# Optimization experiments

Measured on AMD Instinct MI355X. Metric: run time of the kernel, lower is better.

The kernel has to match this reference:

```python
import jax, jax.numpy as jnp
import numpy as np

B, K, N, F_IN, F_OUT, T = 8, 3, 2048, 16, 64, 12


def setup_inputs() -> dict:
    key = jax.random.key(0)
    k1, k2, k3, k4 = jax.random.split(key, 4)
    x = jax.random.normal(k1, (B, N, F_IN, T), dtype=jnp.float32)
    spatial_attention = jax.random.normal(k2, (B, K, N, N), dtype=jnp.float32)
    adj = jax.random.uniform(k3, (N, N), dtype=jnp.float32)  # fusiongraph() output
    Theta = jax.random.normal(k4, (K, F_IN, F_OUT), dtype=jnp.float32) * 0.1
    return {"x": x, "spatial_attention": spatial_attention, "adj": adj, "Theta": Theta}


def _cheb_polynomials(L_tilde, k_order):
    # NOTE: original uses ELEMENTWISE multiply in the recurrence (L_tilde * T_{k-1}),
    # faithfully reproduced here.
    n = L_tilde.shape[0]
    polys = [jnp.eye(n, dtype=L_tilde.dtype), L_tilde]
    for _ in range(2, k_order):
        polys.append(2.0 * L_tilde * polys[-1] - polys[-2])
    return jnp.stack(polys[:k_order], axis=0)  # (K, N, N)


def reference(x, spatial_attention, adj, Theta):
    # Unnormalized graph Laplacian L = D - A (torch_geometric get_laplacian default).
    deg = jnp.sum(adj, axis=1)                      # (N,)
    L_tilde = jnp.diag(deg) - adj                   # (N, N)
    cheb = _cheb_polynomials(L_tilde, K)            # (K, N, N)

    # softmax over dim=1 of each (B,N,N) slice -> axis=2 of (B,K,N,N); time-invariant.
    attn = jax.nn.softmax(spatial_attention, axis=2)  # (B, K, N, N)
    Tka = cheb[None, :, :, :] * attn                  # (B, K, N, N)

    # rhs[b,n,f,t] = sum_m Tka[b,k,m,n] * x[b,m,f,t]; out = rhs @ Theta_k, summed over k.
    out = jnp.einsum('bkmn,bmft,kfo->bnot', Tka, x, Theta)  # (B, N, F_OUT, T)
    return jax.nn.relu(out)
```

## Files before the change

kernel.cpp:

```cpp
#include <hip/hip_runtime.h>


#define NB 8
#define NN 2048
#define FT 192
#define BN 32
#define BM 64
#define LBM 72
#define ZST 33

typedef __attribute__((ext_vector_type(8))) short short8;
typedef __attribute__((ext_vector_type(4))) float f32x4;

__device__ __forceinline__ unsigned short bf16_rne(float f) {
  unsigned u = __float_as_uint(f);
  u += 0x7FFFu + ((u >> 16) & 1u);
  return (unsigned short)(u >> 16);
}

__device__ __forceinline__ void gload_lds16(const float* g, float* l) {
  __builtin_amdgcn_global_load_lds(
      (const __attribute__((address_space(1))) void*)g,
      (__attribute__((address_space(3))) void*)l, 16, 0, 0);
}

__global__ __launch_bounds__(256) void k_deg(const float* __restrict__ adj,
                                             float* __restrict__ deg) {
  const int row = blockIdx.x;
  const float* r = adj + (size_t)row * NN;
  float s = 0.f;
  for (int j = threadIdx.x; j < NN; j += 256) s += r[j];
  for (int off = 32; off; off >>= 1) s += __shfl_down(s, off, 64);
  __shared__ float ls[4];
  if ((threadIdx.x & 63) == 0) ls[threadIdx.x >> 6] = s;
  __syncthreads();
  if (threadIdx.x == 0) deg[row] = ls[0] + ls[1] + ls[2] + ls[3];
}

__global__ __launch_bounds__(192) void k_xt(const float* __restrict__ x,
                                            unsigned short* __restrict__ xT) {
  const int b = blockIdx.y, m0 = blockIdx.x * 32, ft = threadIdx.x;
  const float* src = x + (size_t)b * NN * FT + ft;
  uint4* dst = (uint4*)(xT + ((size_t)b * FT + ft) * NN + m0);
#pragma unroll
  for (int g = 0; g < 4; ++g) {
    unsigned u[4];
#pragma unroll
    for (int j = 0; j < 4; ++j) {
      float lo = src[(size_t)(m0 + g * 8 + 2 * j) * FT];
      float hi = src[(size_t)(m0 + g * 8 + 2 * j + 1) * FT];
      u[j] = (unsigned)bf16_rne(lo) | ((unsigned)bf16_rne(hi) << 16);
    }
    dst[g] = make_uint4(u[0], u[1], u[2], u[3]);
  }
}

__global__ __launch_bounds__(256, 2) void k_fused(
    const float* __restrict__ Sall, const float* __restrict__ adj,
    const float* __restrict__ deg, const unsigned short* __restrict__ xT,
    const float* __restrict__ x, const float* __restrict__ Theta,
    float* __restrict__ out) {
  __shared__ __align__(16) char smem[74752];
  __shared__ float dEs[BN];
  __shared__ float sc[3][BN];

  float* const Sr1 = (float*)smem;
  float* const Sr2 = (float*)(smem + 8192);
  unsigned short* const PtB = (unsigned short*)(smem + 16384);

  const int flat = blockIdx.x + (blockIdx.y << 6);
  const int b = flat & 7;
  const int tile = flat >> 3;
  const int n0 = tile * BN;

  const int t = threadIdx.x;
  const int lane = t & 63, w = t >> 6;
  const int ln = lane & 15, quad = lane >> 4;
  const int col4 = (t & 7) << 2;
  const int rowg = t >> 3;
  const int srow = lane >> 3;
  const int scol = (lane & 7) << 2;

  const float* S0 = Sall + (size_t)b * 3 * NN * NN;
  const float* S1 = S0 + (size_t)NN * NN;
  const float* S2 = S1 + (size_t)NN * NN;
  const unsigned short* xb = xT + (size_t)b * FT * NN;

  const int cdiag = n0 >> 6;
  const float4 dgv = *(const float4*)(deg + n0 + col4);

  const f32x4 zero4 = {0.f, 0.f, 0.f, 0.f};
  f32x4 acc1[2][3], acc2[2][3];
#pragma unroll
  for (int i = 0; i < 2; ++i)
#pragma unroll
    for (int q = 0; q < 3; ++q) {
      acc1[i][q] = zero4;
      acc2[i][q] = zero4;
    }
  float zp0[4] = {0.f, 0.f, 0.f, 0.f};
  float zp1[4] = {0.f, 0.f, 0.f, 0.f};
  float zp2[4] = {0.f, 0.f, 0.f, 0.f};

  auto STAGE = [&](int c) {
    const int m0s = c * BM;
#pragma unroll
    for (int j2 = 0; j2 < 2; ++j2) {
      const int r0 = (w << 4) + (j2 << 3);
      const size_t go = (size_t)(m0s + r0 + srow) * NN + n0 + scol;
      gload_lds16(S1 + go, Sr1 + r0 * BN);
      gload_lds16(S2 + go, Sr2 + r0 * BN);
    }
  };

  auto LOADAV = [&](int c, float4 av[2], float4 sv[2]) {
#pragma unroll
    for (int r = 0; r < 2; ++r) {
      const int gm = c * BM + rowg * 2 + r;
      av[r] = *(const float4*)(adj + (size_t)gm * NN + n0 + col4);
      sv[r] = *(const float4*)(S0 + (size_t)gm * NN + n0 + col4);
    }
  };

  auto PACK = [&](int c, int buf, const float4 av[2], const float4 sv[2]) {
    const bool isd = (c == cdiag);
    unsigned short* P1 = PtB + (size_t)buf * 2304;
    unsigned short* P2 = PtB + (size_t)(2 + buf) * 2304;
    unsigned short q1[2][4], q2[2][4];
    const float dg[4] = {dgv.x, dgv.y, dgv.z, dgv.w};
#pragma unroll
    for (int r = 0; r < 2; ++r) {
      const int lrow = rowg * 2 + r;
      const float4 s1 = *(const float4*)&Sr1[lrow * BN + col4];
      const float4 s2 = *(const float4*)&Sr2[lrow * BN + col4];
      const float se1[4] = {s1.x, s1.y, s1.z, s1.w};
      const float se2[4] = {s2.x, s2.y, s2.z, s2.w};
      const float aa[4] = {av[r].x, av[r].y, av[r].z, av[r].w};
      const float s0e[4] = {sv[r].x, sv[r].y, sv[r].z, sv[r].w};
#pragma unroll
      for (int j = 0; j < 4; ++j) {
        const float e0 = __expf(s0e[j]);
        const float e1 = __expf(se1[j]);
        const float e2 = __expf(se2[j]);
        zp0[j] += e0;
        zp1[j] += e1;
        zp2[j] += e2;
        float c1 = -aa[j];
        float c2 = 2.f * aa[j] * aa[j];
        if (isd) {
          if (c * BM + lrow == n0 + col4 + j) {
            const float L = dg[j] - aa[j];
            c1 = L;
            c2 = 2.f * L * L - 1.f;
            dEs[col4 + j] = e0;
          }
        }
        q1[r][j] = bf16_rne(e1 * c1);
        q2[r][j] = bf16_rne(e2 * c2);
      }
    }
#pragma unroll
    for (int j = 0; j < 4; ++j) {
      const unsigned v1 = (unsigned)q1[0][j] | ((unsigned)q1[1][j] << 16);
      const unsigned v2 = (unsigned)q2[0][j] | ((unsigned)q2[1][j] << 16);
      *(unsigned*)&P1[(col4 + j) * LBM + rowg * 2] = v1;
      *(unsigned*)&P2[(col4 + j) * LBM + rowg * 2] = v2;
    }
  };

  STAGE(0);
  {
    float4 av[2], sv[2];
    LOADAV(0, av, sv);
    asm volatile("s_waitcnt vmcnt(0)" ::: "memory");
    __builtin_amdgcn_sched_barrier(0);
    PACK(0, 0, av, sv);
  }
  __syncthreads();

  for (int c = 0; c < 32; ++c) {
    const int buf = c & 1;
    const bool more = (c < 31);
    const int m0 = c * BM;

    short8 bfr[2][3];
#pragma unroll
    for (int ks2 = 0; ks2 < 2; ++ks2)
#pragma unroll
      for (int q = 0; q < 3; ++q)
        bfr[ks2][q] = *(const short8*)(xb +
            (size_t)(w * 48 + q * 16 + ln) * NN + m0 + ks2 * 32 + quad * 8);
    __builtin_amdgcn_sched_barrier(0);

    float4 avn[2], svn[2];
    if (more) {
      STAGE(c + 1);
      LOADAV(c + 1, avn, svn);
    }
    __builtin_amdgcn_sched_barrier(0);

#pragma unroll
    for (int ks2 = 0; ks2 < 2; ++ks2) {
      short8 a1[2], a2[2];
#pragma unroll
      for (int i = 0; i < 2; ++i) {
        a1[i] = *(const short8*)&PtB[(size_t)buf * 2304 + (i * 16 + ln) * LBM +
                                     ks2 * 32 + quad * 8];
        a2[i] = *(const short8*)&PtB[(size_t)(2 + buf) * 2304 +
                                     (i * 16 + ln) * LBM + ks2 * 32 + quad * 8];
      }
#pragma unroll
      for (int i = 0; i < 2; ++i)
#pragma unroll
        for (int q = 0; q < 3; ++q) {
          acc1[i][q] = __builtin_amdgcn_mfma_f32_16x16x32_bf16(
              a1[i], bfr[ks2][q], acc1[i][q], 0, 0, 0);
          acc2[i][q] = __builtin_amdgcn_mfma_f32_16x16x32_bf16(
              a2[i], bfr[ks2][q], acc2[i][q], 0, 0, 0);
        }
    }

    if (more) {
      asm volatile("s_waitcnt vmcnt(0)" ::: "memory");
      __builtin_amdgcn_sched_barrier(0);
      PACK(c + 1, buf ^ 1, avn, svn);
    }
    __syncthreads();
  }

  float* Zr = (float*)smem;
#pragma unroll
  for (int j = 0; j < 4; ++j) {
    Zr[0 * 32 * ZST + rowg * ZST + col4 + j] = zp0[j];
    Zr[1 * 32 * ZST + rowg * ZST + col4 + j] = zp1[j];
    Zr[2 * 32 * ZST + rowg * ZST + col4 + j] = zp2[j];
  }
  __syncthreads();
  if (t < 96) {
    const int which = t >> 5, n = t & 31;
    float Z = 0.f;
#pragma unroll
    for (int g = 0; g < 32; ++g) Z += Zr[which * 32 * ZST + g * ZST + n];
    sc[which][n] = (which == 0) ? (dEs[n] / Z) : (1.f / Z);
  }
  __syncthreads();

  float* const r1s = (float*)smem;
  float* const r2s = (float*)(smem + 25088);
  float* const xs = (float*)(smem + 50176);
#pragma unroll
  for (int i = 0; i < 2; ++i)
#pragma unroll
    for (int q = 0; q < 3; ++q) {
      const int ft = w * 48 + q * 16 + ln;
#pragma unroll
      for (int r = 0; r < 4; ++r) {
        const int nl = i * 16 + quad * 4 + r;
        r1s[nl * 196 + ft] = acc1[i][q][r];
        r2s[nl * 196 + ft] = acc2[i][q][r];
      }
    }
  for (int l = t; l < 32 * 48; l += 256) {
    const int row = l / 48, c4 = (l % 48) * 4;
    *(float4*)&xs[row * 192 + c4] =
        *(const float4*)(x + ((size_t)b * NN + n0 + row) * FT + c4);
  }
  __syncthreads();

  const int o = t & 63, nl2 = t >> 6;
  float th0[16], th1[16], th2[16];
#pragma unroll
  for (int f = 0; f < 16; ++f) {
    th0[f] = Theta[f * 64 + o];
    th1[f] = Theta[(16 + f) * 64 + o];
    th2[f] = Theta[(32 + f) * 64 + o];
  }
#pragma unroll 1
  for (int ni = 0; ni < 8; ++ni) {
    const int n = ni * 4 + nl2;
    float a0[12], a1[12], a2[12];
#pragma unroll
    for (int e = 0; e < 12; ++e) a0[e] = a1[e] = a2[e] = 0.f;
#pragma unroll
    for (int f = 0; f < 16; ++f) {
      const f32x4* xv = (const f32x4*)&xs[n * 192 + f * 12];
      const f32x4* r1v = (const f32x4*)&r1s[n * 196 + f * 12];
      const f32x4* r2v = (const f32x4*)&r2s[n * 196 + f * 12];
#pragma unroll
      for (int g = 0; g < 3; ++g)
#pragma unroll
        for (int e = 0; e < 4; ++e) {
          a0[g * 4 + e] += th0[f] * xv[g][e];
          a1[g * 4 + e] += th1[f] * r1v[g][e];
          a2[g * 4 + e] += th2[f] * r2v[g][e];
        }
    }
    const float c0 = sc[0][n], rz1 = sc[1][n], rz2 = sc[2][n];
    float4* op = (float4*)(out + (((size_t)b * NN + n0 + n) * 64 + o) * 12);
#pragma unroll
    for (int g = 0; g < 3; ++g) {
      float4 rv;
      rv.x = fmaxf(a0[g * 4 + 0] * c0 + a1[g * 4 + 0] * rz1 + a2[g * 4 + 0] * rz2, 0.f);
      rv.y = fmaxf(a0[g * 4 + 1] * c0 + a1[g * 4 + 1] * rz1 + a2[g * 4 + 1] * rz2, 0.f);
      rv.z = fmaxf(a0[g * 4 + 2] * c0 + a1[g * 4 + 2] * rz1 + a2[g * 4 + 2] * rz2, 0.f);
      rv.w = fmaxf(a0[g * 4 + 3] * c0 + a1[g * 4 + 3] * rz1 + a2[g * 4 + 3] * rz2, 0.f);
      op[g] = rv;
    }
  }
}

extern "C" void kernel_launch(void* const* d_in, const int* in_sizes, int n_in,
                              void* d_out, int out_size, void* d_ws,
                              size_t ws_size, hipStream_t stream) {
  (void)in_sizes;
  (void)n_in;
  (void)out_size;
  const float* x = (const float*)d_in[0];
  const float* s_attn = (const float*)d_in[1];
  const float* adj = (const float*)d_in[2];
  const float* Theta = (const float*)d_in[3];
  float* out = (float*)d_out;
  char* ws = (char*)d_ws;

  const size_t szXT = (size_t)NB * FT * NN * 2;
  const size_t szDeg = NN * 4;
  if (ws_size < szXT + szDeg) return;

  unsigned short* xT = (unsigned short*)ws;
  float* deg = (float*)(ws + szXT);

  hipLaunchKernelGGL(k_deg, dim3(NN), dim3(256), 0, stream, adj, deg);
  hipLaunchKernelGGL(k_xt, dim3(64, NB), dim3(192), 0, stream, x, xT);
  hipLaunchKernelGGL(k_fused, dim3(64, NB), dim3(256), 0, stream, s_attn, adj,
                     deg, xT, x, Theta, out);
}
```

Baseline: 642.8 us.

## Double-buffer staged attention tiles and merge prep kernels into one launch

```diff
diff --git a/kernel.cpp b/kernel.cpp
--- a/kernel.cpp
+++ b/kernel.cpp
@@ -24,34 +24,39 @@
       (__attribute__((address_space(3))) void*)l, 16, 0, 0);
 }
 
-__global__ __launch_bounds__(256) void k_deg(const float* __restrict__ adj,
-                                             float* __restrict__ deg) {
-  const int row = blockIdx.x;
-  const float* r = adj + (size_t)row * NN;
-  float s = 0.f;
-  for (int j = threadIdx.x; j < NN; j += 256) s += r[j];
-  for (int off = 32; off; off >>= 1) s += __shfl_down(s, off, 64);
+__global__ __launch_bounds__(256) void k_prep(const float* __restrict__ adj,
+                                              float* __restrict__ deg,
+                                              const float* __restrict__ x,
+                                              unsigned short* __restrict__ xT) {
   __shared__ float ls[4];
-  if ((threadIdx.x & 63) == 0) ls[threadIdx.x >> 6] = s;
-  __syncthreads();
-  if (threadIdx.x == 0) deg[row] = ls[0] + ls[1] + ls[2] + ls[3];
-}
-
-__global__ __launch_bounds__(192) void k_xt(const float* __restrict__ x,
-                                            unsigned short* __restrict__ xT) {
-  const int b = blockIdx.y, m0 = blockIdx.x * 32, ft = threadIdx.x;
-  const float* src = x + (size_t)b * NN * FT + ft;
-  uint4* dst = (uint4*)(xT + ((size_t)b * FT + ft) * NN + m0);
-#pragma unroll
-  for (int g = 0; g < 4; ++g) {
-    unsigned u[4];
-#pragma unroll
-    for (int j = 0; j < 4; ++j) {
-      float lo = src[(size_t)(m0 + g * 8 + 2 * j) * FT];
-      float hi = src[(size_t)(m0 + g * 8 + 2 * j + 1) * FT];
-      u[j] = (unsigned)bf16_rne(lo) | ((unsigned)bf16_rne(hi) << 16);
-    }
-    dst[g] = make_uint4(u[0], u[1], u[2], u[3]);
+  const int bid = blockIdx.x;
+  if (bid < NN) {
+    const float* r = adj + (size_t)bid * NN;
+    float s = 0.f;
+    for (int j = threadIdx.x; j < NN; j += 256) s += r[j];
+    for (int off = 32; off; off >>= 1) s += __shfl_down(s, off, 64);
+    if ((threadIdx.x & 63) == 0) ls[threadIdx.x >> 6] = s;
+    __syncthreads();
+    if (threadIdx.x == 0) deg[bid] = ls[0] + ls[1] + ls[2] + ls[3];
+  } else {
+    const int xbk = bid - NN;
+    const int b = xbk >> 6, m0 = (xbk & 63) * 32;
+    const int ft = threadIdx.x;
+    if (ft < FT) {
+      const float* src = x + (size_t)b * NN * FT + ft;
+      uint4* dst = (uint4*)(xT + ((size_t)b * FT + ft) * NN + m0);
+#pragma unroll
+      for (int g = 0; g < 4; ++g) {
+        unsigned u[4];
+#pragma unroll
+        for (int j = 0; j < 4; ++j) {
+          float lo = src[(size_t)(m0 + g * 8 + 2 * j) * FT];
+          float hi = src[(size_t)(m0 + g * 8 + 2 * j + 1) * FT];
+          u[j] = (unsigned)bf16_rne(lo) | ((unsigned)bf16_rne(hi) << 16);
+        }
+        dst[g] = make_uint4(u[0], u[1], u[2], u[3]);
+      }
+    }
   }
 }
 
@@ -64,9 +69,11 @@
   __shared__ float dEs[BN];
   __shared__ float sc[3][BN];
 
-  float* const Sr1 = (float*)smem;
-  float* const Sr2 = (float*)(smem + 8192);
-  unsigned short* const PtB = (unsigned short*)(smem + 16384);
+  float* const SrA1 = (float*)smem;
+  float* const SrA2 = (float*)(smem + 8192);
+  float* const SrB1 = (float*)(smem + 16384);
+  float* const SrB2 = (float*)(smem + 24576);
+  unsigned short* const PtB = (unsigned short*)(smem + 32768);
 
   const int flat = blockIdx.x + (blockIdx.y << 6);
   const int b = flat & 7;
@@ -84,7 +91,7 @@
   const float* S0 = Sall + (size_t)b * 3 * NN * NN;
   const float* S1 = S0 + (size_t)NN * NN;
   const float* S2 = S1 + (size_t)NN * NN;
-  const unsigned short* xb = xT + (size_t)b * FT * NN;
+  const unsigned short* xbp = xT + (size_t)b * FT * NN;
 
   const int cdiag = n0 >> 6;
   const float4 dgv = *(const float4*)(deg + n0 + col4);
@@ -102,14 +109,14 @@
   float zp1[4] = {0.f, 0.f, 0.f, 0.f};
   float zp2[4] = {0.f, 0.f, 0.f, 0.f};
 
-  auto STAGE = [&](int c) {
+  auto STAGE = [&](int c, float* d1, float* d2) {
     const int m0s = c * BM;
 #pragma unroll
     for (int j2 = 0; j2 < 2; ++j2) {
       const int r0 = (w << 4) + (j2 << 3);
       const size_t go = (size_t)(m0s + r0 + srow) * NN + n0 + scol;
-      gload_lds16(S1 + go, Sr1 + r0 * BN);
-      gload_lds16(S2 + go, Sr2 + r0 * BN);
+      gload_lds16(S1 + go, d1 + r0 * BN);
+      gload_lds16(S2 + go, d2 + r0 * BN);
     }
   };
 
@@ -122,17 +129,18 @@
     }
   };
 
-  auto PACK = [&](int c, int buf, const float4 av[2], const float4 sv[2]) {
+  auto PACK = [&](int c, int pbuf, const float* R1, const float* R2,
+                  const float4 av[2], const float4 sv[2]) {
     const bool isd = (c == cdiag);
-    unsigned short* P1 = PtB + (size_t)buf * 2304;
-    unsigned short* P2 = PtB + (size_t)(2 + buf) * 2304;
+    unsigned short* P1 = PtB + (size_t)pbuf * 2304;
+    unsigned short* P2 = PtB + (size_t)(2 + pbuf) * 2304;
     unsigned short q1[2][4], q2[2][4];
     const float dg[4] = {dgv.x, dgv.y, dgv.z, dgv.w};
 #pragma unroll
     for (int r = 0; r < 2; ++r) {
       const int lrow = rowg * 2 + r;
-      const float4 s1 = *(const float4*)&Sr1[lrow * BN + col4];
-      const float4 s2 = *(const float4*)&Sr2[lrow * BN + col4];
+      const float4 s1 = *(const float4*)&R1[lrow * BN + col4];
+      const float4 s2 = *(const float4*)&R2[lrow * BN + col4];
       const float se1[4] = {s1.x, s1.y, s1.z, s1.w};
       const float se2[4] = {s2.x, s2.y, s2.z, s2.w};
       const float aa[4] = {av[r].x, av[r].y, av[r].z, av[r].w};
@@ -168,45 +176,25 @@
     }
   };
 
-  STAGE(0);
-  {
-    float4 av[2], sv[2];
-    LOADAV(0, av, sv);
-    asm volatile("s_waitcnt vmcnt(0)" ::: "memory");
-    __builtin_amdgcn_sched_barrier(0);
-    PACK(0, 0, av, sv);
-  }
-  __syncthreads();
-
-  for (int c = 0; c < 32; ++c) {
-    const int buf = c & 1;
-    const bool more = (c < 31);
+  auto BFR = [&](int c, short8 bfr[2][3]) {
     const int m0 = c * BM;
-
-    short8 bfr[2][3];
 #pragma unroll
     for (int ks2 = 0; ks2 < 2; ++ks2)
 #pragma unroll
       for (int q = 0; q < 3; ++q)
-        bfr[ks2][q] = *(const short8*)(xb +
+        bfr[ks2][q] = *(const short8*)(xbp +
             (size_t)(w * 48 + q * 16 + ln) * NN + m0 + ks2 * 32 + quad * 8);
-    __builtin_amdgcn_sched_barrier(0);
-
-    float4 avn[2], svn[2];
-    if (more) {
-      STAGE(c + 1);
-      LOADAV(c + 1, avn, svn);
-    }
-    __builtin_amdgcn_sched_barrier(0);
-
+  };
+
+  auto MFMAh = [&](int pbuf, const short8 bfr[2][3]) {
 #pragma unroll
     for (int ks2 = 0; ks2 < 2; ++ks2) {
       short8 a1[2], a2[2];
 #pragma unroll
       for (int i = 0; i < 2; ++i) {
-        a1[i] = *(const short8*)&PtB[(size_t)buf * 2304 + (i * 16 + ln) * LBM +
+        a1[i] = *(const short8*)&PtB[(size_t)pbuf * 2304 + (i * 16 + ln) * LBM +
                                      ks2 * 32 + quad * 8];
-        a2[i] = *(const short8*)&PtB[(size_t)(2 + buf) * 2304 +
+        a2[i] = *(const short8*)&PtB[(size_t)(2 + pbuf) * 2304 +
                                      (i * 16 + ln) * LBM + ks2 * 32 + quad * 8];
       }
 #pragma unroll
@@ -219,13 +207,53 @@
               a2[i], bfr[ks2][q], acc2[i][q], 0, 0, 0);
         }
     }
-
-    if (more) {
-      asm volatile("s_waitcnt vmcnt(0)" ::: "memory");
-      __builtin_amdgcn_sched_barrier(0);
-      PACK(c + 1, buf ^ 1, avn, svn);
-    }
-    __syncthreads();
+  };
+
+  float4 avA[2], svA[2], avB[2], svB[2];
+
+  STAGE(0, SrA1, SrA2);
+  LOADAV(0, avA, svA);
+  asm volatile("s_waitcnt vmcnt(0)" ::: "memory");
+  __builtin_amdgcn_sched_barrier(0);
+  PACK(0, 0, SrA1, SrA2, avA, svA);
+  STAGE(1, SrB1, SrB2);
+  LOADAV(1, avB, svB);
+  asm volatile("s_waitcnt lgkmcnt(0)" ::: "memory");
+  __builtin_amdgcn_s_barrier();
+
+  for (int c2 = 0; c2 < 32; c2 += 2) {
+    {
+      short8 bfr[2][3];
+      BFR(c2, bfr);
+      __builtin_amdgcn_sched_barrier(0);
+      if (c2 + 2 < 32) {
+        STAGE(c2 + 2, SrA1, SrA2);
+        LOADAV(c2 + 2, avA, svA);
+      }
+      __builtin_amdgcn_sched_barrier(0);
+      MFMAh(0, bfr);
+      asm volatile("s_waitcnt vmcnt(8)" ::: "memory");
+      __builtin_amdgcn_sched_barrier(0);
+      PACK(c2 + 1, 1, SrB1, SrB2, avB, svB);
+      asm volatile("s_waitcnt lgkmcnt(0)" ::: "memory");
+      __builtin_amdgcn_s_barrier();
+    }
+    {
+      short8 bfr[2][3];
+      BFR(c2 + 1, bfr);
+      __builtin_amdgcn_sched_barrier(0);
+      if (c2 + 3 < 32) {
+        STAGE(c2 + 3, SrB1, SrB2);
+        LOADAV(c2 + 3, avB, svB);
+      }
+      __builtin_amdgcn_sched_barrier(0);
+      MFMAh(1, bfr);
+      asm volatile("s_waitcnt vmcnt(8)" ::: "memory");
+      __builtin_amdgcn_sched_barrier(0);
+      if (c2 + 2 < 32) PACK(c2 + 2, 0, SrA1, SrA2, avA, svA);
+      asm volatile("s_waitcnt lgkmcnt(0)" ::: "memory");
+      __builtin_amdgcn_s_barrier();
+    }
   }
 
   float* Zr = (float*)smem;
@@ -329,8 +357,8 @@
   unsigned short* xT = (unsigned short*)ws;
   float* deg = (float*)(ws + szXT);
 
-  hipLaunchKernelGGL(k_deg, dim3(NN), dim3(256), 0, stream, adj, deg);
-  hipLaunchKernelGGL(k_xt, dim3(64, NB), dim3(192), 0, stream, x, xT);
+  hipLaunchKernelGGL(k_prep, dim3(NN + 512), dim3(256), 0, stream, adj, deg, x,
+                     xT);
   hipLaunchKernelGGL(k_fused, dim3(64, NB), dim3(256), 0, stream, s_attn, adj,
                      deg, xT, x, Theta, out);
 }
```

Result: no change. 654.0 us (+1.7%).
